# Kernel optimization log

Hardware: AMD Instinct MI355X
Metric: run time of the kernel (lower is better)

The kernel has to match this reference:

```python
import jax, jax.numpy as jnp
import numpy as np

IN_N, OUT_N, KER, FEAT, HID = 50, 10, 10, 66, 256
VLEN = KER + OUT_N            # 20
VSEQ = IN_N - KER - OUT_N + 1 # 31
IF = 2 * VLEN                 # 40, GCN input feature size
NBLK = 12                     # 6 GC blocks x 2 graph convs
BN_EPS = 1e-5


def get_dct_matrix(N):
    k = np.arange(N)[:, None]
    i = np.arange(N)[None, :]
    w = np.full((N, 1), np.sqrt(2.0 / N))
    w[0, 0] = np.sqrt(1.0 / N)
    dct = (w * np.cos(np.pi * (i + 0.5) * k / N)).astype(np.float32)
    idct = np.linalg.inv(dct).astype(np.float32)
    return jnp.array(dct), jnp.array(idct)


def conv1d(x, w, b):
    # x: [B, Cin, T], w: [Cout, Cin, K]
    y = jax.lax.conv_general_dilated(x, w, (1,), 'VALID',
                                     dimension_numbers=('NCH', 'OIH', 'NCH'))
    return y + b[None, :, None]


def _forward(x, q_w1, q_b1, q_w2, q_b2, k_w1, k_b1, k_w2, k_b2,
             gin_w, gin_att, gin_b, bn_in_g, bn_in_b,
             blk_w, blk_att, blk_b, blk_bn_g, blk_bn_b,
             gout_w, gout_att, gout_b):
    dct, idct = get_dct_matrix(VLEN)
    B = x.shape[0]
    x = x[:, :IN_N]
    # q/k conv nets (Conv1d k=6 -> ReLU -> Conv1d k=5 -> ReLU)
    qs = jnp.transpose(x[:, IN_N - OUT_N:], (0, 2, 1))   # [B, FEAT, OUT_N]
    ksrc = jnp.transpose(x[:, :IN_N - OUT_N], (0, 2, 1)) # [B, FEAT, IN_N-OUT_N]
    q = jax.nn.relu(conv1d(jax.nn.relu(conv1d(qs, q_w1, q_b1)), q_w2, q_b2))    # [B, HID, 1]
    k = jax.nn.relu(conv1d(jax.nn.relu(conv1d(ksrc, k_w1, k_b1)), k_w2, k_b2))  # [B, HID, VSEQ]
    scores = jnp.einsum('bhq,bhs->bqs', q, k)            # [B, 1, VSEQ]
    att = scores[:, 0, :] / jnp.sum(scores, axis=-1)     # sum-normalized, [B, VSEQ]
    # overlapping windowed value gather + DCT
    vidx = np.arange(VLEN)[None, :] + np.arange(VSEQ)[:, None]
    value_mat = x[:, vidx, :]                             # [B, VSEQ, VLEN, FEAT]
    value_dct = jnp.einsum('bslf,lm->bsfm', value_mat, dct)  # [B, VSEQ, FEAT, VLEN]
    vdct_r = value_dct.reshape(B, FEAT, VSEQ, VLEN)       # raw reshape, as in torch source
    att_final = jnp.einsum('bs,bfsl->bfl', att, vdct_r)   # [B, FEAT, VLEN]
    # padded query (last KER frames + OUT_N repeats of last frame) in DCT space
    pidx = np.concatenate([np.arange(IN_N - KER, IN_N), np.full(OUT_N, IN_N - 1)])
    padded_query = jnp.einsum('bfl,lm->bfm', jnp.transpose(x[:, pidx], (0, 2, 1)), dct)
    gcn_inp = jnp.concatenate([padded_query, att_final], axis=2)  # [B, FEAT, IF]

    def gc(h, w, a, b):  # graph conv with learnable adjacency over FEAT nodes
        return jnp.einsum('nm,bmf->bnf', a, h @ w) + b

    def bn(h, g, beta):  # eval-mode BatchNorm1d over flattened [FEAT*feat] dim
        hf = h.reshape(B, -1)
        return ((hf / jnp.sqrt(1.0 + BN_EPS)) * g + beta).reshape(h.shape)

    y = jnp.tanh(bn(gc(gcn_inp, gin_w, gin_att, gin_b), bn_in_g, bn_in_b))
    for i in range(0, NBLK, 2):
        res = y
        y = jnp.tanh(bn(gc(y, blk_w[i], blk_att[i], blk_b[i]), blk_bn_g[i], blk_bn_b[i]))
        y = jnp.tanh(bn(gc(y, blk_w[i + 1], blk_att[i + 1], blk_b[i + 1]), blk_bn_g[i + 1], blk_bn_b[i + 1]))
        y = y + res
    gcn_out = gc(y, gout_w, gout_att, gout_b) + gcn_inp   # [B, FEAT, IF]
    return jnp.einsum('bfl,lm->bfm', gcn_out[:, :, :VLEN], idct)  # [B, FEAT, VLEN]


def setup_inputs():
    key = jax.random.key(0)
    ks = jax.random.split(key, 12)
    B = 2048
    s = 0.05
    NN = FEAT * HID
    return {
        'x': jax.random.normal(ks[0], (B, IN_N, FEAT), jnp.float32),
        'q_w1': jax.random.normal(ks[1], (HID, FEAT, 6), jnp.float32) * s,
        'q_b1': jnp.zeros((HID,), jnp.float32),
        'q_w2': jax.random.normal(ks[2], (HID, HID, 5), jnp.float32) * s,
        'q_b2': jnp.zeros((HID,), jnp.float32),
        'k_w1': jax.random.normal(ks[3], (HID, FEAT, 6), jnp.float32) * s,
        'k_b1': jnp.zeros((HID,), jnp.float32),
        'k_w2': jax.random.normal(ks[4], (HID, HID, 5), jnp.float32) * s,
        'k_b2': jnp.zeros((HID,), jnp.float32),
        'gin_w': jax.random.normal(ks[5], (IF, HID), jnp.float32) * s,
        'gin_att': jax.random.normal(ks[6], (FEAT, FEAT), jnp.float32) * s,
        'gin_b': jnp.zeros((HID,), jnp.float32),
        'bn_in_g': jnp.ones((NN,), jnp.float32),
        'bn_in_b': jnp.zeros((NN,), jnp.float32),
        'blk_w': jax.random.normal(ks[7], (NBLK, HID, HID), jnp.float32) * s,
        'blk_att': jax.random.normal(ks[8], (NBLK, FEAT, FEAT), jnp.float32) * s,
        'blk_b': jnp.zeros((NBLK, HID), jnp.float32),
        'blk_bn_g': jnp.ones((NBLK, NN), jnp.float32),
        'blk_bn_b': jnp.zeros((NBLK, NN), jnp.float32),
        'gout_w': jax.random.normal(ks[9], (HID, IF), jnp.float32) * s,
        'gout_att': jax.random.normal(ks[10], (FEAT, FEAT), jnp.float32) * s,
        'gout_b': jnp.zeros((IF,), jnp.float32),
    }


def reference(x, q_w1, q_b1, q_w2, q_b2, k_w1, k_b1, k_w2, k_b2,
              gin_w, gin_att, gin_b, bn_in_g, bn_in_b,
              blk_w, blk_att, blk_b, blk_bn_g, blk_bn_b,
              gout_w, gout_att, gout_b):
    return _forward(x, q_w1, q_b1, q_w2, q_b2, k_w1, k_b1, k_w2, k_b2,
                    gin_w, gin_att, gin_b, bn_in_g, bn_in_b,
                    blk_w, blk_att, blk_b, blk_bn_g, blk_bn_b,
                    gout_w, gout_att, gout_b)
```

## Files before the change

### kernel.cpp

```cpp
#include <hip/hip_runtime.h>
#include <math.h>

typedef unsigned short u16;
typedef unsigned int u32;

#define FEATN 66
#define HIDN 256
#define NNDIM 16896
#define INVS 0.9999950000374998f
#ifndef M_PI
#define M_PI 3.14159265358979323846
#endif

typedef __attribute__((ext_vector_type(4))) float f32x4;
typedef __attribute__((ext_vector_type(2))) float f32x2;
typedef __attribute__((ext_vector_type(8))) short s16x8;

__device__ __forceinline__ u32 bf_rne(float x) {
    u32 i = __float_as_uint(x);
    return (i + 0x7fffu + ((i >> 16) & 1u)) >> 16;
}

__global__ void dct_kernel(float* __restrict__ dct) {
    int t = threadIdx.x;
    if (t < 400) {
        int k = t / 20, i = t % 20;
        double w = (k == 0) ? sqrt(1.0 / 20.0) : sqrt(2.0 / 20.0);
        dct[t] = (float)(w * cos(M_PI * (i + 0.5) * k / 20.0));
    }
}

__global__ __launch_bounds__(256) void pack_w_kernel(
    const float* __restrict__ blk_w, u16* __restrict__ wh, u16* __restrict__ wl) {
    int gid = blockIdx.x * 256 + threadIdx.x;
    if (gid >= 12 * 65536) return;
    int layer = gid >> 16, rmd = gid & 65535;
    int ks = rmd >> 13;
    int r2 = rmd & 8191;
    int ct = r2 >> 9;
    int r3 = r2 & 511;
    int lane = r3 >> 3, j = r3 & 7;
    int k = ks * 32 + (lane >> 4) * 8 + j;
    int n = ct * 16 + (lane & 15);
    float v = blk_w[(size_t)layer * 65536 + k * 256 + n];
    u32 rhi = bf_rne(v);
    float hif = __uint_as_float(rhi << 16);
    u32 rlo = bf_rne(v - hif);
    wh[gid] = (u16)rhi;
    wl[gid] = (u16)rlo;
}

__global__ __launch_bounds__(256) void pack_w2_kernel(
    const float* __restrict__ w2, u16* __restrict__ wh, u16* __restrict__ wl) {
    int gid = blockIdx.x * 256 + threadIdx.x;
    if (gid >= 40 * 16 * 512) return;
    int ks = gid >> 13;
    int r2 = gid & 8191;
    int ct = r2 >> 9;
    int r3 = r2 & 511;
    int lane = r3 >> 3, j = r3 & 7;
    int k = ks * 32 + (lane >> 4) * 8 + j;
    int n = ct * 16 + (lane & 15);
    int h = k & 255, t = k >> 8;
    float v = w2[(size_t)n * 1280 + h * 5 + t];
    u32 rhi = bf_rne(v);
    float hif = __uint_as_float(rhi << 16);
    u32 rlo = bf_rne(v - hif);
    wh[gid] = (u16)rhi;
    wl[gid] = (u16)rlo;
}

__global__ __launch_bounds__(256) void pack_w1_kernel(
    const float* __restrict__ w1, u16* __restrict__ wh, u16* __restrict__ wl) {
    int gid = blockIdx.x * 256 + threadIdx.x;
    if (gid >= 13 * 16 * 512) return;
    int ks = gid >> 13;
    int r2 = gid & 8191;
    int ct = r2 >> 9;
    int r3 = r2 & 511;
    int lane = r3 >> 3, j = r3 & 7;
    int k = ks * 32 + (lane >> 4) * 8 + j;
    int n = ct * 16 + (lane & 15);
    float v = 0.f;
    if (k < 396) {
        int f = k % 66, t = k / 66;
        v = w1[(size_t)n * 396 + f * 6 + t];
    }
    u32 rhi = bf_rne(v);
    float hif = __uint_as_float(rhi << 16);
    u32 rlo = bf_rne(v - hif);
    wh[gid] = (u16)rhi;
    wl[gid] = (u16)rlo;
}

__global__ __launch_bounds__(256) void pack_att_kernel(
    const float* __restrict__ blk_att, u16* __restrict__ ah, u16* __restrict__ al) {
    int gid = blockIdx.x * 256 + threadIdx.x;
    if (gid >= 12 * 7680) return;
    int layer = gid / 7680, rem = gid % 7680;
    int rt = rem / 1536, rem2 = rem % 1536;
    int ks = rem2 / 512, r3 = rem2 % 512;
    int lane = r3 >> 3, j = r3 & 7;
    int n = rt * 16 + (lane & 15);
    int k = ks * 32 + (lane >> 4) * 8 + j;
    float v = (n < 66 && k < 66) ? blk_att[(size_t)layer * 4356 + n * 66 + k] : 0.f;
    u32 rhi = bf_rne(v);
    float hif = __uint_as_float(rhi << 16);
    u32 rlo = bf_rne(v - hif);
    ah[gid] = (u16)rhi;
    al[gid] = (u16)rlo;
}

__global__ __launch_bounds__(256, 1) void conv1_mfma_kernel(
    const float* __restrict__ x,
    const u16* __restrict__ whq, const u16* __restrict__ wlq,
    const u16* __restrict__ whk, const u16* __restrict__ wlk,
    const float* __restrict__ bq, const float* __restrict__ bk,
    float* __restrict__ q1, float* __restrict__ k1, int Cc, int nbq) {
    __shared__ u16 Ah[64 * 136];
    __shared__ u16 Al[64 * 136];
    const int tid = threadIdx.x;
    const int lane = tid & 63, wid = tid >> 6;
    const int m = lane & 15, quad = lane >> 4;
    const bool isq = ((int)blockIdx.x < nbq);
    const int bid = isq ? (int)blockIdx.x : ((int)blockIdx.x - nbq);
    const int rows = isq ? Cc * 5 : Cc * 35;
    const int row0 = bid * 64;
    const u16* wh = isq ? whq : whk;
    const u16* wl = isq ? wlq : wlk;
    const float* bias = isq ? bq : bk;
    float* out = isq ? q1 : k1;

    const int cq = tid & 31;
    const int r0t = (tid >> 5) * 8;
    int rbc[8]; bool vld[8];
#pragma unroll
    for (int s = 0; s < 8; s++) {
        int grow = row0 + r0t + s;
        int rbv;
        if (isq) { int bb = grow / 5;  rbv = bb * 3300 + 2640 + (grow - bb * 5) * 66; }
        else     { int bb = grow / 35; rbv = bb * 3300 + (grow - bb * 35) * 66; }
        vld[s] = (grow < rows);
        rbc[s] = vld[s] ? rbv : 0;
    }

    f32x4 acc[4][4];
#pragma unroll
    for (int rt = 0; rt < 4; rt++)
#pragma unroll
        for (int ct = 0; ct < 4; ct++) acc[rt][ct] = (f32x4)0.f;

    f32x2 ldA[16], ldB[16];

    auto LOADP = [&](f32x2* dst, int ph) {
        const int off = ph * 128 + cq * 4;
        const bool kok = (off < 396);
        const int o = kok ? off : 0;
#pragma unroll
        for (int s = 0; s < 8; s++) {
            const float* p = x + rbc[s] + o;
            dst[2 * s]     = *(const f32x2*)p;
            dst[2 * s + 1] = *(const f32x2*)(p + 2);
        }
    };
    auto STOREP = [&](const f32x2* src, int ph) {
        const bool kok = (ph * 128 + cq * 4) < 396;
#pragma unroll
        for (int s = 0; s < 8; s++) {
            float v0 = src[2 * s][0], v1 = src[2 * s][1];
            float v2 = src[2 * s + 1][0], v3 = src[2 * s + 1][1];
            if (!vld[s] || !kok) { v0 = v1 = v2 = v3 = 0.f; }
            u32 H0 = bf_rne(v0), H1 = bf_rne(v1), H2 = bf_rne(v2), H3 = bf_rne(v3);
            u32 L0 = bf_rne(v0 - __uint_as_float(H0 << 16));
            u32 L1 = bf_rne(v1 - __uint_as_float(H1 << 16));
            u32 L2 = bf_rne(v2 - __uint_as_float(H2 << 16));
            u32 L3 = bf_rne(v3 - __uint_as_float(H3 << 16));
            int o = (r0t + s) * 136 + cq * 4;
            *(uint2*)&Ah[o] = make_uint2(H0 | (H1 << 16), H2 | (H3 << 16));
            *(uint2*)&Al[o] = make_uint2(L0 | (L1 << 16), L2 | (L3 << 16));
        }
    };
    auto MFMAP = [&](int ph) {
#pragma unroll
        for (int ks = 0; ks < 4; ks++) {
            const int ksg = ph * 4 + ks;
            if (ksg >= 13) break;
            s16x8 ahf[4], alf[4], bhf[4], blf[4];
#pragma unroll
            for (int rt = 0; rt < 4; rt++) {
                int o2 = (rt * 16 + m) * 136 + ks * 32 + quad * 8;
                ahf[rt] = *(const s16x8*)&Ah[o2];
                alf[rt] = *(const s16x8*)&Al[o2];
            }
#pragma unroll
            for (int ct = 0; ct < 4; ct++) {
                size_t boff = ((size_t)(ksg * 16 + wid * 4 + ct)) * 512 + lane * 8;
                bhf[ct] = *(const s16x8*)&wh[boff];
                blf[ct] = *(const s16x8*)&wl[boff];
            }
#pragma unroll
            for (int rt = 0; rt < 4; rt++) {
#pragma unroll
                for (int ct = 0; ct < 4; ct++) {
                    acc[rt][ct] = __builtin_amdgcn_mfma_f32_16x16x32_bf16(
                        ahf[rt], bhf[ct], acc[rt][ct], 0, 0, 0);
                    acc[rt][ct] = __builtin_amdgcn_mfma_f32_16x16x32_bf16(
                        ahf[rt], blf[ct], acc[rt][ct], 0, 0, 0);
                    acc[rt][ct] = __builtin_amdgcn_mfma_f32_16x16x32_bf16(
                        alf[rt], bhf[ct], acc[rt][ct], 0, 0, 0);
                }
            }
        }
    };

    LOADP(ldA, 0);
    for (int ph = 0; ph < 4; ph += 2) {
        __syncthreads();
        STOREP(ldA, ph);
        LOADP(ldB, ph + 1);
        __syncthreads();
        MFMAP(ph);
        __syncthreads();
        STOREP(ldB, ph + 1);
        if (ph + 2 < 4) LOADP(ldA, ph + 2);
        __syncthreads();
        MFMAP(ph + 1);
    }

#pragma unroll
    for (int rt = 0; rt < 4; rt++) {
        int rb2 = row0 + rt * 16 + quad * 4;
#pragma unroll
        for (int r = 0; r < 4; r++) {
            int grow = rb2 + r;
            if (grow >= rows) continue;
#pragma unroll
            for (int ct = 0; ct < 4; ct++) {
                int f = wid * 64 + ct * 16 + m;
                float v = acc[rt][ct][r] + bias[f];
                out[(size_t)grow * 256 + f] = fmaxf(v, 0.f);
            }
        }
    }
}

__global__ __launch_bounds__(256, 1) void conv2_mfma_kernel(
    const float* __restrict__ Aq, const float* __restrict__ Ak,
    const u16* __restrict__ whq, const u16* __restrict__ wlq,
    const u16* __restrict__ whk, const u16* __restrict__ wlk,
    const float* __restrict__ bq, const float* __restrict__ bk,
    float* __restrict__ q2, float* __restrict__ k2, int Cc, int nbq) {
    __shared__ u16 Ah[64 * 136];
    __shared__ u16 Al[64 * 136];
    const int tid = threadIdx.x;
    const int lane = tid & 63, wid = tid >> 6;
    const int m = lane & 15, quad = lane >> 4;
    const bool isq = ((int)blockIdx.x < nbq);
    const int bid = isq ? (int)blockIdx.x : ((int)blockIdx.x - nbq);
    const int rows = isq ? Cc : Cc * 31;
    const int row0 = bid * 64;
    const float* Asrc = isq ? Aq : Ak;
    const u16* wh = isq ? whq : whk;
    const u16* wl = isq ? wlq : wlk;
    const float* bias = isq ? bq : bk;
    float* out = isq ? q2 : k2;

    const int cq = tid & 31;
    const int r0t = (tid >> 5) * 8;
    int rbc[8]; bool vld[8];
#pragma unroll
    for (int s = 0; s < 8; s++) {
        int grow = row0 + r0t + s;
        int rbv;
        if (isq) rbv = grow * 1280;
        else { int bb = grow / 31; rbv = bb * 8960 + (grow - bb * 31) * 256; }
        vld[s] = (grow < rows);
        rbc[s] = vld[s] ? rbv : 0;
    }

    f32x4 acc[4][4];
#pragma unroll
    for (int rt = 0; rt < 4; rt++)
#pragma unroll
        for (int ct = 0; ct < 4; ct++) acc[rt][ct] = (f32x4)0.f;

    f32x4 ldA[8], ldB[8];

    auto LOADP = [&](f32x4* dst, int ph) {
        const int off = ph * 128 + cq * 4;
#pragma unroll
        for (int s = 0; s < 8; s++)
            dst[s] = *(const f32x4*)(Asrc + rbc[s] + off);
    };
    auto STOREP = [&](const f32x4* src) {
#pragma unroll
        for (int s = 0; s < 8; s++) {
            f32x4 v = src[s];
            if (!vld[s]) v = (f32x4)0.f;
            u32 H0 = bf_rne(v[0]), H1 = bf_rne(v[1]), H2 = bf_rne(v[2]), H3 = bf_rne(v[3]);
            u32 L0 = bf_rne(v[0] - __uint_as_float(H0 << 16));
            u32 L1 = bf_rne(v[1] - __uint_as_float(H1 << 16));
            u32 L2 = bf_rne(v[2] - __uint_as_float(H2 << 16));
            u32 L3 = bf_rne(v[3] - __uint_as_float(H3 << 16));
            int o = (r0t + s) * 136 + cq * 4;
            *(uint2*)&Ah[o] = make_uint2(H0 | (H1 << 16), H2 | (H3 << 16));
            *(uint2*)&Al[o] = make_uint2(L0 | (L1 << 16), L2 | (L3 << 16));
        }
    };
    auto MFMAP = [&](int ph) {
#pragma unroll
        for (int ks = 0; ks < 4; ks++) {
            const int ksg = ph * 4 + ks;
            s16x8 ahf[4], alf[4], bhf[4], blf[4];
#pragma unroll
            for (int rt = 0; rt < 4; rt++) {
                int o2 = (rt * 16 + m) * 136 + ks * 32 + quad * 8;
                ahf[rt] = *(const s16x8*)&Ah[o2];
                alf[rt] = *(const s16x8*)&Al[o2];
            }
#pragma unroll
            for (int ct = 0; ct < 4; ct++) {
                size_t boff = ((size_t)(ksg * 16 + wid * 4 + ct)) * 512 + lane * 8;
                bhf[ct] = *(const s16x8*)&wh[boff];
                blf[ct] = *(const s16x8*)&wl[boff];
            }
#pragma unroll
            for (int rt = 0; rt < 4; rt++) {
#pragma unroll
                for (int ct = 0; ct < 4; ct++) {
                    acc[rt][ct] = __builtin_amdgcn_mfma_f32_16x16x32_bf16(
                        ahf[rt], bhf[ct], acc[rt][ct], 0, 0, 0);
                    acc[rt][ct] = __builtin_amdgcn_mfma_f32_16x16x32_bf16(
                        ahf[rt], blf[ct], acc[rt][ct], 0, 0, 0);
                    acc[rt][ct] = __builtin_amdgcn_mfma_f32_16x16x32_bf16(
                        alf[rt], bhf[ct], acc[rt][ct], 0, 0, 0);
                }
            }
        }
    };

    LOADP(ldA, 0);
    for (int ph = 0; ph < 10; ph += 2) {
        __syncthreads();
        STOREP(ldA);
        LOADP(ldB, ph + 1);
        __syncthreads();
        MFMAP(ph);
        __syncthreads();
        STOREP(ldB);
        if (ph + 2 < 10) LOADP(ldA, ph + 2);
        __syncthreads();
        MFMAP(ph + 1);
    }

#pragma unroll
    for (int rt = 0; rt < 4; rt++) {
        int rb2 = row0 + rt * 16 + quad * 4;
#pragma unroll
        for (int r = 0; r < 4; r++) {
            int grow = rb2 + r;
            if (grow >= rows) continue;
#pragma unroll
            for (int ct = 0; ct < 4; ct++) {
                int f = wid * 64 + ct * 16 + m;
                float v = acc[rt][ct][r] + bias[f];
                out[(size_t)grow * 256 + f] = fmaxf(v, 0.f);
            }
        }
    }
}

__global__ void att_kernel(const float* __restrict__ q2, const float* __restrict__ k2,
                           float* __restrict__ att) {
    __shared__ float q2s[256];
    const int b = blockIdx.x, tid = threadIdx.x;
    for (int i = tid; i < 256; i += 64) q2s[i] = q2[(size_t)b * 256 + i];
    __syncthreads();
    float sc = 0.f;
    if (tid < 31) {
        const f32x4* kp = (const f32x4*)(k2 + (size_t)b * 7936 + tid * 256);
        for (int c = 0; c < 64; c++) {
            f32x4 kv = kp[c];
            sc = fmaf(q2s[c * 4 + 0], kv[0], sc);
            sc = fmaf(q2s[c * 4 + 1], kv[1], sc);
            sc = fmaf(q2s[c * 4 + 2], kv[2], sc);
            sc = fmaf(q2s[c * 4 + 3], kv[3], sc);
        }
    }
    float tot = sc;
#pragma unroll
    for (int off = 1; off < 64; off <<= 1) tot += __shfl_xor(tot, off);
    if (tid < 31) att[(size_t)b * 32 + tid] = (tot != 0.f) ? (sc / tot) : 0.f;
}

__global__ __launch_bounds__(256) void gcn_inp_kernel(
    const float* __restrict__ x, const float* __restrict__ att,
    const float* __restrict__ dct, float* __restrict__ ginp) {
    __shared__ float xs[3300];
    __shared__ float dctS[400];
    __shared__ float attS[31];
    const int b = blockIdx.x, tid = threadIdx.x;
    const float* xb = x + (size_t)b * 3300;
    for (int idx = tid; idx < 3300; idx += 256) xs[idx] = xb[idx];
    for (int idx = tid; idx < 400; idx += 256) dctS[idx] = dct[idx];
    if (tid < 31) attS[tid] = att[(size_t)b * 32 + tid];
    __syncthreads();
    for (int idx = tid; idx < 2640; idx += 256) {
        int n = idx / 40, l = idx - n * 40;
        float acc = 0.f;
        if (l < 20) {
#pragma unroll
            for (int l1 = 0; l1 < 20; l1++) {
                int r = (l1 < 10) ? (40 + l1) : 49;
                acc = fmaf(xs[r * FEATN + n], dctS[l1 * 20 + l], acc);
            }
        } else {
            int j = l - 20;
            for (int s2 = 0; s2 < 31; s2++) {
                int mx = n * 31 + s2;
                int s1 = mx / 66, f1 = mx - s1 * 66;
                float inner = 0.f;
#pragma unroll
                for (int l1 = 0; l1 < 20; l1++)
                    inner = fmaf(xs[(s1 + l1) * FEATN + f1], dctS[l1 * 20 + j], inner);
                acc = fmaf(attS[s2], inner, acc);
            }
        }
        ginp[(size_t)b * 2640 + idx] = acc;
    }
}

__global__ __launch_bounds__(256) void attmul_gin_kernel(
    const float* __restrict__ ginp, const float* __restrict__ attm,
    float* __restrict__ out) {
    __shared__ float gS[2640];
    __shared__ float attS[4356];
    const int b = blockIdx.x, tid = threadIdx.x;
    for (int idx = tid; idx < 2640; idx += 256) gS[idx] = ginp[(size_t)b * 2640 + idx];
    for (int idx = tid; idx < 4356; idx += 256) attS[idx] = attm[idx];
    __syncthreads();
    for (int idx = tid; idx < 2640; idx += 256) {
        int n = idx / 40, l = idx - n * 40;
        float acc = 0.f;
        for (int mm = 0; mm < 66; mm++)
            acc = fmaf(attS[n * 66 + mm], gS[mm * 40 + l], acc);
        out[(size_t)b * 2640 + idx] = acc;
    }
}

__global__ __launch_bounds__(256) void attmul_kernel(
    const float* __restrict__ S, const float* __restrict__ attm,
    float* __restrict__ out) {
    __shared__ float Ss[66 * 64];
    __shared__ float attS[4356];
    const int b = blockIdx.x, tid = threadIdx.x;
    for (int idx = tid; idx < 4356; idx += 256) attS[idx] = attm[idx];
    const float* Sb = S + (size_t)b * NNDIM;
    float* ob = out + (size_t)b * NNDIM;
    const int fl = tid & 63, ng = tid >> 6;
    for (int f0 = 0; f0 < 256; f0 += 64) {
        __syncthreads();
        for (int idx = tid; idx < 66 * 64; idx += 256) {
            int mm = idx >> 6, j = idx & 63;
            Ss[idx] = Sb[mm * 256 + f0 + j];
        }
        __syncthreads();
        for (int n = ng; n < 66; n += 4) {
            float acc = 0.f;
            const float* ar = &attS[n * 66];
#pragma unroll 11
            for (int mm = 0; mm < 66; mm++)
                acc = fmaf(ar[mm], Ss[(mm << 6) + fl], acc);
            ob[n * 256 + f0 + fl] = acc;
        }
    }
}

template <int K, bool RES>
__global__ __launch_bounds__(256) void wmul_kernel(
    const float* __restrict__ Z, const float* __restrict__ W,
    const float* __restrict__ bias, const float* __restrict__ g,
    const float* __restrict__ beta, const float* __restrict__ res,
    float* __restrict__ out, int rows) {
    __shared__ float As[32 * K];
    const int tid = threadIdx.x;
    const size_t row0 = (size_t)blockIdx.x * 32;
    for (int idx = tid; idx < 32 * K; idx += 256) {
        int r = (int)row0 + idx / K;
        As[idx] = (r < rows) ? Z[row0 * K + idx] : 0.f;
    }
    __syncthreads();
    const int fq = tid & 63, rg = tid >> 6;
    float acc[8][4];
#pragma unroll
    for (int r = 0; r < 8; r++)
#pragma unroll
        for (int c = 0; c < 4; c++) acc[r][c] = 0.f;
    for (int i = 0; i < K; i += 4) {
        float w0[4], w1[4], w2[4], w3[4];
#pragma unroll
        for (int fi = 0; fi < 4; fi++) {
            w0[fi] = W[(size_t)(i + 0) * HIDN + fi * 64 + fq];
            w1[fi] = W[(size_t)(i + 1) * HIDN + fi * 64 + fq];
            w2[fi] = W[(size_t)(i + 2) * HIDN + fi * 64 + fq];
            w3[fi] = W[(size_t)(i + 3) * HIDN + fi * 64 + fq];
        }
#pragma unroll
        for (int rr = 0; rr < 8; rr++) {
            const float4 a = *(const float4*)&As[(rg * 8 + rr) * K + i];
#pragma unroll
            for (int fi = 0; fi < 4; fi++) {
                acc[rr][fi] = fmaf(a.x, w0[fi], acc[rr][fi]);
                acc[rr][fi] = fmaf(a.y, w1[fi], acc[rr][fi]);
                acc[rr][fi] = fmaf(a.z, w2[fi], acc[rr][fi]);
                acc[rr][fi] = fmaf(a.w, w3[fi], acc[rr][fi]);
            }
        }
    }
#pragma unroll
    for (int rr = 0; rr < 8; rr++) {
        int r = (int)row0 + rg * 8 + rr;
        if (r >= rows) continue;
        int n = r % 66;
#pragma unroll
        for (int fi = 0; fi < 4; fi++) {
            int f = fi * 64 + fq;
            float v = (acc[rr][fi] + bias[f]) * INVS;
            v = tanhf(fmaf(v, g[n * 256 + f], beta[n * 256 + f]));
            if (RES) v += res[(size_t)r * 256 + f];
            out[(size_t)r * 256 + f] = v;
        }
    }
}

__global__ __launch_bounds__(256, 1) void trunk_kernel(
    float* __restrict__ Y,
    const u16* __restrict__ wpk_hi, const u16* __restrict__ wpk_lo,
    const u16* __restrict__ atA_hi, const u16* __restrict__ atA_lo,
    const float* __restrict__ blk_b,
    const float* __restrict__ bn_g, const float* __restrict__ bn_b) {
    __shared__ u16 Ainh[80 * 264];
    __shared__ u16 Ainl[80 * 264];
    __shared__ u16 Ubh[16 * 64 * 8];
    __shared__ u16 Ubl[16 * 64 * 8];
    const int tid = threadIdx.x;
    const int lane = tid & 63, wid = tid >> 6;
    const int m = lane & 15, quad = lane >> 4;
    const int b = blockIdx.x;
    float* Yb = Y + (size_t)b * NNDIM;

    for (int idx = tid; idx < 8448; idx += 256) {
        int r = idx >> 7, c2 = (idx & 127) * 2;
        float2 yv = *(const float2*)&Yb[r * 256 + c2];
        u32 h0 = bf_rne(yv.x), h1 = bf_rne(yv.y);
        u32 l0 = bf_rne(yv.x - __uint_as_float(h0 << 16));
        u32 l1 = bf_rne(yv.y - __uint_as_float(h1 << 16));
        *(u32*)&Ainh[r * 264 + c2] = h0 | (h1 << 16);
        *(u32*)&Ainl[r * 264 + c2] = l0 | (l1 << 16);
    }
    for (int idx = tid; idx < 14 * 264; idx += 256) {
        Ainh[66 * 264 + idx] = 0; Ainl[66 * 264 + idx] = 0;
    }
    for (int idx = tid; idx < 8192; idx += 256) { Ubh[idx] = 0; Ubl[idx] = 0; }

    float carry[5][4][4];
#pragma unroll
    for (int rt = 0; rt < 5; rt++)
#pragma unroll
        for (int r = 0; r < 4; r++) {
            int n = rt * 16 + quad * 4 + r;
#pragma unroll
            for (int ct = 0; ct < 4; ct++) {
                int f = wid * 64 + ct * 16 + m;
                carry[rt][r][ct] = (n < 66) ? Yb[n * 256 + f] : 0.f;
            }
        }
    __syncthreads();

    for (int L = 0; L < 12; L++) {
        const u16* wh  = wpk_hi + (size_t)L * 65536;
        const u16* wl  = wpk_lo + (size_t)L * 65536;
        const u16* ath = atA_hi + (size_t)L * 7680;
        const u16* atl = atA_lo + (size_t)L * 7680;
        const float* bias = blk_b + (size_t)L * 256;
        const float* g    = bn_g + (size_t)L * NNDIM;
        const float* beta = bn_b + (size_t)L * NNDIM;
        const bool RES = (L & 1);

        f32x4 acc[5][4];
#pragma unroll
        for (int rt = 0; rt < 5; rt++)
#pragma unroll
            for (int ct = 0; ct < 4; ct++) acc[rt][ct] = (f32x4)0.f;

        s16x8 pbh[4], pbl[4];
#pragma unroll
        for (int ct = 0; ct < 4; ct++) {
            size_t boff = ((size_t)(wid * 4 + ct)) * 512 + lane * 8;
            pbh[ct] = *(const s16x8*)&wh[boff];
            pbl[ct] = *(const s16x8*)&wl[boff];
        }
#pragma unroll
        for (int ks = 0; ks < 8; ks++) {
            s16x8 nbh[4], nbl[4];
            if (ks < 7) {
#pragma unroll
                for (int ct = 0; ct < 4; ct++) {
                    size_t boff = ((size_t)((ks + 1) * 16 + wid * 4 + ct)) * 512 + lane * 8;
                    nbh[ct] = *(const s16x8*)&wh[boff];
                    nbl[ct] = *(const s16x8*)&wl[boff];
                }
            }
            s16x8 ahf[5], alf[5];
#pragma unroll
            for (int rt = 0; rt < 5; rt++) {
                int o2 = (rt * 16 + m) * 264 + ks * 32 + quad * 8;
                ahf[rt] = *(const s16x8*)&Ainh[o2];
                alf[rt] = *(const s16x8*)&Ainl[o2];
            }
#pragma unroll
            for (int rt = 0; rt < 5; rt++) {
#pragma unroll
                for (int ct = 0; ct < 4; ct++) {
                    acc[rt][ct] = __builtin_amdgcn_mfma_f32_16x16x32_bf16(
                        ahf[rt], pbh[ct], acc[rt][ct], 0, 0, 0);
                    acc[rt][ct] = __builtin_amdgcn_mfma_f32_16x16x32_bf16(
                        ahf[rt], pbl[ct], acc[rt][ct], 0, 0, 0);
                    acc[rt][ct] = __builtin_amdgcn_mfma_f32_16x16x32_bf16(
                        alf[rt], pbh[ct], acc[rt][ct], 0, 0, 0);
                }
            }
            if (ks < 7) {
#pragma unroll
                for (int ct = 0; ct < 4; ct++) { pbh[ct] = nbh[ct]; pbl[ct] = nbl[ct]; }
            }
        }

        f32x4 acc2[5][4];
#pragma unroll
        for (int rt = 0; rt < 5; rt++)
#pragma unroll
            for (int ct = 0; ct < 4; ct++) acc2[rt][ct] = (f32x4)0.f;

#pragma unroll
        for (int ksf = 0; ksf < 3; ksf++) {
            s16x8 afh[5], afl[5];
#pragma unroll
            for (int rt = 0; rt < 5; rt++) {
                size_t aoff = ((size_t)(rt * 3 + ksf)) * 512 + lane * 8;
                afh[rt] = *(const s16x8*)&ath[aoff];
                afl[rt] = *(const s16x8*)&atl[aoff];
            }
#pragma unroll
            for (int rr = 0; rr < 2; rr++) {
                const int rt = ksf * 2 + rr;
                if (rt > 4) continue;
                const int R0 = rt * 16 + quad * 4;
                const int quadf = (R0 >> 3) & 3;
                const int jb = R0 & 7;
#pragma unroll
                for (int ct = 0; ct < 4; ct++) {
                    const int ctg = wid * 4 + ct;
                    const int base = (ctg * 64 + quadf * 16 + m) * 8 + jb;
                    float v0 = acc[rt][ct][0], v1 = acc[rt][ct][1];
                    float v2 = acc[rt][ct][2], v3 = acc[rt][ct][3];
                    u32 H0 = bf_rne(v0), H1 = bf_rne(v1), H2 = bf_rne(v2), H3 = bf_rne(v3);
                    u32 L0 = bf_rne(v0 - __uint_as_float(H0 << 16));
                    u32 L1 = bf_rne(v1 - __uint_as_float(H1 << 16));
                    u32 L2 = bf_rne(v2 - __uint_as_float(H2 << 16));
                    u32 L3 = bf_rne(v3 - __uint_as_float(H3 << 16));
                    *(uint2*)&Ubh[base] = make_uint2(H0 | (H1 << 16), H2 | (H3 << 16));
                    *(uint2*)&Ubl[base] = make_uint2(L0 | (L1 << 16), L2 | (L3 << 16));
                }
            }
            s16x8 ubh[4], ubl[4];
#pragma unroll
            for (int ct = 0; ct < 4; ct++) {
                int uoff = ((wid * 4 + ct) * 64 + lane) * 8;
                ubh[ct] = *(const s16x8*)&Ubh[uoff];
                ubl[ct] = *(const s16x8*)&Ubl[uoff];
            }
#pragma unroll
            for (int rt = 0; rt < 5; rt++) {
#pragma unroll
                for (int ct = 0; ct < 4; ct++) {
                    acc2[rt][ct] = __builtin_amdgcn_mfma_f32_16x16x32_bf16(
                        afh[rt], ubh[ct], acc2[rt][ct], 0, 0, 0);
                    acc2[rt][ct] = __builtin_amdgcn_mfma_f32_16x16x32_bf16(
                        afh[rt], ubl[ct], acc2[rt][ct], 0, 0, 0);
                    acc2[rt][ct] = __builtin_amdgcn_mfma_f32_16x16x32_bf16(
                        afl[rt], ubh[ct], acc2[rt][ct], 0, 0, 0);
                }
            }
        }

        __syncthreads();
#pragma unroll
        for (int rt = 0; rt < 5; rt++) {
            const int nb = rt * 16 + quad * 4;
#pragma unroll
            for (int r = 0; r < 4; r++) {
                const int n = nb + r;
                if (n >= 66) continue;
#pragma unroll
                for (int ct = 0; ct < 4; ct++) {
                    const int f = wid * 64 + ct * 16 + m;
                    float v = (acc2[rt][ct][r] + bias[f]) * INVS;
                    v = tanhf(fmaf(v, g[n * 256 + f], beta[n * 256 + f]));
                    if (RES) { v += carry[rt][r][ct]; carry[rt][r][ct] = v; }
                    u32 H = bf_rne(v);
                    u32 Lo = bf_rne(v - __uint_as_float(H << 16));
                    Ainh[n * 264 + f] = (u16)H;
                    Ainl[n * 264 + f] = (u16)Lo;
                    if (L == 11) Yb[n * 256 + f] = v;
                }
            }
        }
        __syncthreads();
    }
}

__global__ __launch_bounds__(256) void final_kernel(
    const float* __restrict__ T, const float* __restrict__ gw,
    const float* __restrict__ gb, const float* __restrict__ gi,
    const float* __restrict__ dct, float* __restrict__ out) {
    __shared__ float Zt[66 * 64];
    __shared__ float gwS[256 * 20];
    __shared__ float goS[1320];
    __shared__ float dctS[400];
    const int b = blockIdx.x, tid = threadIdx.x;
    for (int idx = tid; idx < 5120; idx += 256) {
        int i = idx / 20, l = idx - i * 20;
        gwS[idx] = gw[i * 40 + l];
    }
    for (int idx = tid; idx < 400; idx += 256) dctS[idx] = dct[idx];
    for (int idx = tid; idx < 1320; idx += 256) {
        int n = idx / 20, l = idx - n * 20;
        goS[idx] = gb[l] + gi[(size_t)b * 2640 + n * 40 + l];
    }
    for (int t = 0; t < 4; t++) {
        __syncthreads();
        for (int idx = tid; idx < 66 * 64; idx += 256) {
            int mm = idx >> 6, j = idx & 63;
            Zt[idx] = T[(size_t)b * NNDIM + mm * 256 + t * 64 + j];
        }
        __syncthreads();
        for (int idx = tid; idx < 1320; idx += 256) {
            int n = idx / 20, l = idx - n * 20;
            float acc = 0.f;
#pragma unroll
            for (int j = 0; j < 64; j++)
                acc = fmaf(Zt[(n << 6) + j], gwS[(t * 64 + j) * 20 + l], acc);
            goS[idx] += acc;
        }
    }
    __syncthreads();
    for (int idx = tid; idx < 1320; idx += 256) {
        int n = idx / 20, mm = idx - n * 20;
        float o = 0.f;
#pragma unroll
        for (int l = 0; l < 20; l++)
            o = fmaf(goS[n * 20 + l], dctS[mm * 20 + l], o);
        out[(size_t)b * 1320 + idx] = o;
    }
}

extern "C" void kernel_launch(void* const* d_in, const int* in_sizes, int n_in,
                              void* d_out, int out_size, void* d_ws, size_t ws_size,
                              hipStream_t stream) {
    const float* x        = (const float*)d_in[0];
    const float* q_w1     = (const float*)d_in[1];
    const float* q_b1     = (const float*)d_in[2];
    const float* q_w2     = (const float*)d_in[3];
    const float* q_b2     = (const float*)d_in[4];
    const float* k_w1     = (const float*)d_in[5];
    const float* k_b1     = (const float*)d_in[6];
    const float* k_w2     = (const float*)d_in[7];
    const float* k_b2     = (const float*)d_in[8];
    const float* gin_w    = (const float*)d_in[9];
    const float* gin_att  = (const float*)d_in[10];
    const float* gin_b    = (const float*)d_in[11];
    const float* bn_in_g  = (const float*)d_in[12];
    const float* bn_in_b  = (const float*)d_in[13];
    const float* blk_w    = (const float*)d_in[14];
    const float* blk_att  = (const float*)d_in[15];
    const float* blk_b    = (const float*)d_in[16];
    const float* blk_bn_g = (const float*)d_in[17];
    const float* blk_bn_b = (const float*)d_in[18];
    const float* gout_w   = (const float*)d_in[19];
    const float* gout_att = (const float*)d_in[20];
    const float* gout_b   = (const float*)d_in[21];
    float* out = (float*)d_out;

    const int B = in_sizes[0] / 3300;

    float* dctb = (float*)d_ws;
    u16* wpk_hi = (u16*)((char*)d_ws + 4096);
    u16* wpk_lo = wpk_hi + 12 * 65536;
    u16* w2q_hi = wpk_lo + 12 * 65536;
    u16* w2q_lo = w2q_hi + 40 * 16 * 512;
    u16* w2k_hi = w2q_lo + 40 * 16 * 512;
    u16* w2k_lo = w2k_hi + 40 * 16 * 512;
    u16* atA_hi = w2k_lo + 40 * 16 * 512;
    u16* atA_lo = atA_hi + 12 * 7680;
    u16* w1q_hi = atA_lo + 12 * 7680;
    u16* w1q_lo = w1q_hi + 13 * 16 * 512;
    u16* w1k_hi = w1q_lo + 13 * 16 * 512;
    u16* w1k_lo = w1k_hi + 13 * 16 * 512;
    const size_t BASE = 4096 + (size_t)2 * 12 * 65536 * 2 + (size_t)4 * 40 * 16 * 512 * 2
                        + (size_t)2 * 12 * 7680 * 2 + (size_t)4 * 13 * 16 * 512 * 2;
    char* R = (char*)d_ws + BASE;
    size_t avail = (ws_size > BASE) ? (ws_size - BASE) : 0;

    const size_t PER_B = 36720ull * 4ull;
    int C = B;
    while (C > 1 && (size_t)C * PER_B > avail) C >>= 1;

    dct_kernel<<<1, 512, 0, stream>>>(dctb);
    pack_w_kernel<<<(12 * 65536) / 256, 256, 0, stream>>>(blk_w, wpk_hi, wpk_lo);
    pack_w2_kernel<<<(40 * 16 * 512) / 256, 256, 0, stream>>>(q_w2, w2q_hi, w2q_lo);
    pack_w2_kernel<<<(40 * 16 * 512) / 256, 256, 0, stream>>>(k_w2, w2k_hi, w2k_lo);
    pack_att_kernel<<<(12 * 7680) / 256, 256, 0, stream>>>(blk_att, atA_hi, atA_lo);
    pack_w1_kernel<<<(13 * 16 * 512) / 256, 256, 0, stream>>>(q_w1, w1q_hi, w1q_lo);
    pack_w1_kernel<<<(13 * 16 * 512) / 256, 256, 0, stream>>>(k_w1, w1k_hi, w1k_lo);

    for (int c0 = 0; c0 < B; c0 += C) {
        const int Cc = (B - c0 < C) ? (B - c0) : C;
        const float* xc = x + (size_t)c0 * 3300;
        float* outc = out + (size_t)c0 * 1320;

        float* Yb  = (float*)R;
        float* Tb  = Yb + (size_t)C * 16896;
        float* gib = Tb + (size_t)C * 16896;
        float* ab  = gib + (size_t)C * 2640;
        float* q2b = ab + (size_t)C * 32;
        float* k1b = Yb;
        float* k2b = Tb;
        float* q1b = gib;

        const int c1q = (Cc * 5 + 63) / 64, c1k = (Cc * 35 + 63) / 64;
        conv1_mfma_kernel<<<c1q + c1k, 256, 0, stream>>>(
            xc, w1q_hi, w1q_lo, w1k_hi, w1k_lo, q_b1, k_b1, q1b, k1b, Cc, c1q);
        const int c2q = (Cc + 63) / 64, c2k = (Cc * 31 + 63) / 64;
        conv2_mfma_kernel<<<c2q + c2k, 256, 0, stream>>>(
            q1b, k1b, w2q_hi, w2q_lo, w2k_hi, w2k_lo, q_b2, k_b2, q2b, k2b, Cc, c2q);
        att_kernel<<<Cc, 64, 0, stream>>>(q2b, k2b, ab);
        gcn_inp_kernel<<<Cc, 256, 0, stream>>>(xc, ab, dctb, gib);

        const int rows = Cc * FEATN;
        const int g32 = (rows + 31) / 32;

        attmul_gin_kernel<<<Cc, 256, 0, stream>>>(gib, gin_att, Tb);
        wmul_kernel<40, false><<<g32, 256, 0, stream>>>(Tb, gin_w, gin_b,
                                                        bn_in_g, bn_in_b, nullptr, Yb, rows);
        trunk_kernel<<<Cc, 256, 0, stream>>>(Yb, wpk_hi, wpk_lo, atA_hi, atA_lo,
                                             blk_b, blk_bn_g, blk_bn_b);
        attmul_kernel<<<Cc, 256, 0, stream>>>(Yb, gout_att, Tb);
        final_kernel<<<Cc, 256, 0, stream>>>(Tb, gout_w, gout_b, gib, dctb, outc);
    }
}
```

Measured before the change: 3.900 ms.

## Split trunk kernel across 16 waves with one column tile per wave

Raises the trunk kernel block from 256 to 1024 threads so each wave computes a single 16-column tile instead of four. Accumulator and fragment register arrays shrink by a factor of four, and the adjacency operand loads move into the inner loop. The intent is better latency hiding and MFMA issue across more waves per CU, at the cost of reloading shared-memory activation fragments once per column tile rather than reusing them across four tiles.

```diff
diff --git a/kernel.cpp b/kernel.cpp
--- a/kernel.cpp
+++ b/kernel.cpp
@@ -533,7 +533,7 @@
     }
 }
 
-__global__ __launch_bounds__(256, 1) void trunk_kernel(
+__global__ __launch_bounds__(1024, 1) void trunk_kernel(
     float* __restrict__ Y,
     const u16* __restrict__ wpk_hi, const u16* __restrict__ wpk_lo,
     const u16* __restrict__ atA_hi, const u16* __restrict__ atA_lo,
@@ -544,12 +544,13 @@
     __shared__ u16 Ubh[16 * 64 * 8];
     __shared__ u16 Ubl[16 * 64 * 8];
     const int tid = threadIdx.x;
-    const int lane = tid & 63, wid = tid >> 6;
+    const int lane = tid & 63, wv = tid >> 6;
     const int m = lane & 15, quad = lane >> 4;
     const int b = blockIdx.x;
     float* Yb = Y + (size_t)b * NNDIM;
-
-    for (int idx = tid; idx < 8448; idx += 256) {
+    const int f = wv * 16 + m;
+
+    for (int idx = tid; idx < 8448; idx += 1024) {
         int r = idx >> 7, c2 = (idx & 127) * 2;
         float2 yv = *(const float2*)&Yb[r * 256 + c2];
         u32 h0 = bf_rne(yv.x), h1 = bf_rne(yv.y);
@@ -558,22 +559,18 @@
         *(u32*)&Ainh[r * 264 + c2] = h0 | (h1 << 16);
         *(u32*)&Ainl[r * 264 + c2] = l0 | (l1 << 16);
     }
-    for (int idx = tid; idx < 14 * 264; idx += 256) {
+    for (int idx = tid; idx < 14 * 264; idx += 1024) {
         Ainh[66 * 264 + idx] = 0; Ainl[66 * 264 + idx] = 0;
     }
-    for (int idx = tid; idx < 8192; idx += 256) { Ubh[idx] = 0; Ubl[idx] = 0; }
-
-    float carry[5][4][4];
+    for (int idx = tid; idx < 8192; idx += 1024) { Ubh[idx] = 0; Ubl[idx] = 0; }
+
+    float carry[5][4];
 #pragma unroll
     for (int rt = 0; rt < 5; rt++)
 #pragma unroll
         for (int r = 0; r < 4; r++) {
             int n = rt * 16 + quad * 4 + r;
-#pragma unroll
-            for (int ct = 0; ct < 4; ct++) {
-                int f = wid * 64 + ct * 16 + m;
-                carry[rt][r][ct] = (n < 66) ? Yb[n * 256 + f] : 0.f;
-            }
+            carry[rt][r] = (n < 66) ? Yb[n * 256 + f] : 0.f;
         }
     __syncthreads();
 
@@ -587,70 +584,38 @@
         const float* beta = bn_b + (size_t)L * NNDIM;
         const bool RES = (L & 1);
 
-        f32x4 acc[5][4];
-#pragma unroll
-        for (int rt = 0; rt < 5; rt++)
-#pragma unroll
-            for (int ct = 0; ct < 4; ct++) acc[rt][ct] = (f32x4)0.f;
-
-        s16x8 pbh[4], pbl[4];
-#pragma unroll
-        for (int ct = 0; ct < 4; ct++) {
-            size_t boff = ((size_t)(wid * 4 + ct)) * 512 + lane * 8;
-            pbh[ct] = *(const s16x8*)&wh[boff];
-            pbl[ct] = *(const s16x8*)&wl[boff];
-        }
+        f32x4 acc[5];
+#pragma unroll
+        for (int rt = 0; rt < 5; rt++) acc[rt] = (f32x4)0.f;
+
+        s16x8 pbh = *(const s16x8*)&wh[(size_t)wv * 512 + lane * 8];
+        s16x8 pbl = *(const s16x8*)&wl[(size_t)wv * 512 + lane * 8];
 #pragma unroll
         for (int ks = 0; ks < 8; ks++) {
-            s16x8 nbh[4], nbl[4];
+            s16x8 nbh, nbl;
             if (ks < 7) {
-#pragma unroll
-                for (int ct = 0; ct < 4; ct++) {
-                    size_t boff = ((size_t)((ks + 1) * 16 + wid * 4 + ct)) * 512 + lane * 8;
-                    nbh[ct] = *(const s16x8*)&wh[boff];
-                    nbl[ct] = *(const s16x8*)&wl[boff];
-                }
-            }
-            s16x8 ahf[5], alf[5];
+                size_t boff = ((size_t)((ks + 1) * 16 + wv)) * 512 + lane * 8;
+                nbh = *(const s16x8*)&wh[boff];
+                nbl = *(const s16x8*)&wl[boff];
+            }
 #pragma unroll
             for (int rt = 0; rt < 5; rt++) {
                 int o2 = (rt * 16 + m) * 264 + ks * 32 + quad * 8;
-                ahf[rt] = *(const s16x8*)&Ainh[o2];
-                alf[rt] = *(const s16x8*)&Ainl[o2];
-            }
-#pragma unroll
-            for (int rt = 0; rt < 5; rt++) {
-#pragma unroll
-                for (int ct = 0; ct < 4; ct++) {
-                    acc[rt][ct] = __builtin_amdgcn_mfma_f32_16x16x32_bf16(
-                        ahf[rt], pbh[ct], acc[rt][ct], 0, 0, 0);
-                    acc[rt][ct] = __builtin_amdgcn_mfma_f32_16x16x32_bf16(
-                        ahf[rt], pbl[ct], acc[rt][ct], 0, 0, 0);
-                    acc[rt][ct] = __builtin_amdgcn_mfma_f32_16x16x32_bf16(
-                        alf[rt], pbh[ct], acc[rt][ct], 0, 0, 0);
-                }
-            }
-            if (ks < 7) {
-#pragma unroll
-                for (int ct = 0; ct < 4; ct++) { pbh[ct] = nbh[ct]; pbl[ct] = nbl[ct]; }
-            }
-        }
-
-        f32x4 acc2[5][4];
-#pragma unroll
-        for (int rt = 0; rt < 5; rt++)
-#pragma unroll
-            for (int ct = 0; ct < 4; ct++) acc2[rt][ct] = (f32x4)0.f;
+                s16x8 ahf = *(const s16x8*)&Ainh[o2];
+                s16x8 alf = *(const s16x8*)&Ainl[o2];
+                acc[rt] = __builtin_amdgcn_mfma_f32_16x16x32_bf16(ahf, pbh, acc[rt], 0, 0, 0);
+                acc[rt] = __builtin_amdgcn_mfma_f32_16x16x32_bf16(ahf, pbl, acc[rt], 0, 0, 0);
+                acc[rt] = __builtin_amdgcn_mfma_f32_16x16x32_bf16(alf, pbh, acc[rt], 0, 0, 0);
+            }
+            if (ks < 7) { pbh = nbh; pbl = nbl; }
+        }
+
+        f32x4 acc2[5];
+#pragma unroll
+        for (int rt = 0; rt < 5; rt++) acc2[rt] = (f32x4)0.f;
 
 #pragma unroll
         for (int ksf = 0; ksf < 3; ksf++) {
-            s16x8 afh[5], afl[5];
-#pragma unroll
-            for (int rt = 0; rt < 5; rt++) {
-                size_t aoff = ((size_t)(rt * 3 + ksf)) * 512 + lane * 8;
-                afh[rt] = *(const s16x8*)&ath[aoff];
-                afl[rt] = *(const s16x8*)&atl[aoff];
-            }
 #pragma unroll
             for (int rr = 0; rr < 2; rr++) {
                 const int rt = ksf * 2 + rr;
@@ -658,39 +623,27 @@
                 const int R0 = rt * 16 + quad * 4;
                 const int quadf = (R0 >> 3) & 3;
                 const int jb = R0 & 7;
-#pragma unroll
-                for (int ct = 0; ct < 4; ct++) {
-                    const int ctg = wid * 4 + ct;
-                    const int base = (ctg * 64 + quadf * 16 + m) * 8 + jb;
-                    float v0 = acc[rt][ct][0], v1 = acc[rt][ct][1];
-                    float v2 = acc[rt][ct][2], v3 = acc[rt][ct][3];
-                    u32 H0 = bf_rne(v0), H1 = bf_rne(v1), H2 = bf_rne(v2), H3 = bf_rne(v3);
-                    u32 L0 = bf_rne(v0 - __uint_as_float(H0 << 16));
-                    u32 L1 = bf_rne(v1 - __uint_as_float(H1 << 16));
-                    u32 L2 = bf_rne(v2 - __uint_as_float(H2 << 16));
-                    u32 L3 = bf_rne(v3 - __uint_as_float(H3 << 16));
-                    *(uint2*)&Ubh[base] = make_uint2(H0 | (H1 << 16), H2 | (H3 << 16));
-                    *(uint2*)&Ubl[base] = make_uint2(L0 | (L1 << 16), L2 | (L3 << 16));
-                }
-            }
-            s16x8 ubh[4], ubl[4];
-#pragma unroll
-            for (int ct = 0; ct < 4; ct++) {
-                int uoff = ((wid * 4 + ct) * 64 + lane) * 8;
-                ubh[ct] = *(const s16x8*)&Ubh[uoff];
-                ubl[ct] = *(const s16x8*)&Ubl[uoff];
-            }
+                const int base = (wv * 64 + quadf * 16 + m) * 8 + jb;
+                float v0 = acc[rt][0], v1 = acc[rt][1];
+                float v2 = acc[rt][2], v3 = acc[rt][3];
+                u32 H0 = bf_rne(v0), H1 = bf_rne(v1), H2 = bf_rne(v2), H3 = bf_rne(v3);
+                u32 L0 = bf_rne(v0 - __uint_as_float(H0 << 16));
+                u32 L1 = bf_rne(v1 - __uint_as_float(H1 << 16));
+                u32 L2 = bf_rne(v2 - __uint_as_float(H2 << 16));
+                u32 L3 = bf_rne(v3 - __uint_as_float(H3 << 16));
+                *(uint2*)&Ubh[base] = make_uint2(H0 | (H1 << 16), H2 | (H3 << 16));
+                *(uint2*)&Ubl[base] = make_uint2(L0 | (L1 << 16), L2 | (L3 << 16));
+            }
+            s16x8 ubh = *(const s16x8*)&Ubh[(wv * 64 + lane) * 8];
+            s16x8 ubl = *(const s16x8*)&Ubl[(wv * 64 + lane) * 8];
 #pragma unroll
             for (int rt = 0; rt < 5; rt++) {
-#pragma unroll
-                for (int ct = 0; ct < 4; ct++) {
-                    acc2[rt][ct] = __builtin_amdgcn_mfma_f32_16x16x32_bf16(
-                        afh[rt], ubh[ct], acc2[rt][ct], 0, 0, 0);
-                    acc2[rt][ct] = __builtin_amdgcn_mfma_f32_16x16x32_bf16(
-                        afh[rt], ubl[ct], acc2[rt][ct], 0, 0, 0);
-                    acc2[rt][ct] = __builtin_amdgcn_mfma_f32_16x16x32_bf16(
-                        afl[rt], ubh[ct], acc2[rt][ct], 0, 0, 0);
-                }
+                size_t aoff = ((size_t)(rt * 3 + ksf)) * 512 + lane * 8;
+                s16x8 afh = *(const s16x8*)&ath[aoff];
+                s16x8 afl = *(const s16x8*)&atl[aoff];
+                acc2[rt] = __builtin_amdgcn_mfma_f32_16x16x32_bf16(afh, ubh, acc2[rt], 0, 0, 0);
+                acc2[rt] = __builtin_amdgcn_mfma_f32_16x16x32_bf16(afh, ubl, acc2[rt], 0, 0, 0);
+                acc2[rt] = __builtin_amdgcn_mfma_f32_16x16x32_bf16(afl, ubh, acc2[rt], 0, 0, 0);
             }
         }
 
@@ -702,18 +655,14 @@
             for (int r = 0; r < 4; r++) {
                 const int n = nb + r;
                 if (n >= 66) continue;
-#pragma unroll
-                for (int ct = 0; ct < 4; ct++) {
-                    const int f = wid * 64 + ct * 16 + m;
-                    float v = (acc2[rt][ct][r] + bias[f]) * INVS;
-                    v = tanhf(fmaf(v, g[n * 256 + f], beta[n * 256 + f]));
-                    if (RES) { v += carry[rt][r][ct]; carry[rt][r][ct] = v; }
-                    u32 H = bf_rne(v);
-                    u32 Lo = bf_rne(v - __uint_as_float(H << 16));
-                    Ainh[n * 264 + f] = (u16)H;
-                    Ainl[n * 264 + f] = (u16)Lo;
-                    if (L == 11) Yb[n * 256 + f] = v;
-                }
+                float v = (acc2[rt][r] + bias[f]) * INVS;
+                v = tanhf(fmaf(v, g[n * 256 + f], beta[n * 256 + f]));
+                if (RES) { v += carry[rt][r]; carry[rt][r] = v; }
+                u32 H = bf_rne(v);
+                u32 Lo = bf_rne(v - __uint_as_float(H << 16));
+                Ainh[n * 264 + f] = (u16)H;
+                Ainl[n * 264 + f] = (u16)Lo;
+                if (L == 11) Yb[n * 256 + f] = v;
             }
         }
         __syncthreads();
@@ -853,8 +802,8 @@
         attmul_gin_kernel<<<Cc, 256, 0, stream>>>(gib, gin_att, Tb);
         wmul_kernel<40, false><<<g32, 256, 0, stream>>>(Tb, gin_w, gin_b,
                                                         bn_in_g, bn_in_b, nullptr, Yb, rows);
-        trunk_kernel<<<Cc, 256, 0, stream>>>(Yb, wpk_hi, wpk_lo, atA_hi, atA_lo,
-                                             blk_b, blk_bn_g, blk_bn_b);
+        trunk_kernel<<<Cc, 1024, 0, stream>>>(Yb, wpk_hi, wpk_lo, atA_hi, atA_lo,
+                                              blk_b, blk_bn_g, blk_bn_b);
         attmul_kernel<<<Cc, 256, 0, stream>>>(Yb, gout_att, Tb);
         final_kernel<<<Cc, 256, 0, stream>>>(Tb, gout_w, gout_b, gib, dctb, outc);
     }
```

Result: slower. 4.421 ms (+13.4%).
